# Performance work log

Hardware: AMD Instinct MI355X
Metric: run time of the kernel (lower is better)

The kernel has to match this reference:

```python
import jax, jax.numpy as jnp
import numpy as np

B, H, L, K = 4096, 2048, 16384, 32

def setup_inputs() -> dict:
    key = jax.random.key(0)
    k1, k2, k3 = jax.random.split(key, 3)
    x = jax.random.normal(k1, (B, H), dtype=jnp.float32)
    W_enc = jax.random.normal(k2, (L, H), dtype=jnp.float32) * (1.0 / np.sqrt(H))
    W_dec = jax.random.normal(k3, (H, L), dtype=jnp.float32)
    # normalize_decoder(): unit norm along dim=0 (hidden axis), per latent column
    W_dec = W_dec / jnp.linalg.norm(W_dec, axis=0, keepdims=True)
    return {"x": x, "W_enc": W_enc, "W_dec": W_dec, "topk": K}

def reference(x, W_enc, W_dec, topk):
    # encoder: z = relu(x @ W_enc^T)   [B, L]
    z_pre = jnp.einsum('bh,lh->bl', x, W_enc)
    z_relu = jax.nn.relu(z_pre)
    # top-k along last dim, scatter values into zeros (sparse latent code)
    vals, idx = jax.lax.top_k(z_relu, topk)            # [B, K]
    rows = jnp.arange(z_relu.shape[0])[:, None]        # [B, 1]
    z = jnp.zeros_like(z_relu).at[rows, idx].set(vals)  # [B, L]
    # decoder: x_hat = z @ W_dec^T    [B, H]
    x_hat = jnp.einsum('bl,hl->bh', z, W_dec)
    return (x_hat, z)
```

## Files before the change

kernel.cpp:

```cpp
#include <hip/hip_runtime.h>

#define B_ROWS 4096
#define H_DIM  2048
#define L_DIM  16384
#define TOPK   32
#define CAND_CAP 512
#define AMBIG_CAP 128
#define BAND 0.06f
#define ZP_STRIDE (2 * L_DIM)

typedef __attribute__((ext_vector_type(8))) short bf16x8;
typedef __attribute__((ext_vector_type(4))) float f32x4;

__device__ __forceinline__ unsigned short f32_to_bf16(float f) {
  unsigned int u = __float_as_uint(f);
  u += 0x7FFFu + ((u >> 16) & 1u);
  return (unsigned short)(u >> 16);
}
__device__ __forceinline__ float bf16_to_f32(unsigned short h) {
  return __uint_as_float(((unsigned int)h) << 16);
}

__device__ __forceinline__ void gload_lds16(const void* g, void* l) {
  __builtin_amdgcn_global_load_lds(
      (const __attribute__((address_space(1))) unsigned int*)g,
      (__attribute__((address_space(3))) unsigned int*)l, 16, 0, 0);
}

__global__ __launch_bounds__(256) void k_convert(const float* __restrict__ src,
                                                 unsigned short* __restrict__ dst, int n4) {
  int i = blockIdx.x * 256 + threadIdx.x;
  if (i < n4) {
    float4 v = ((const float4*)src)[i];
    ushort4 o;
    o.x = f32_to_bf16(v.x); o.y = f32_to_bf16(v.y);
    o.z = f32_to_bf16(v.z); o.w = f32_to_bf16(v.w);
    ((ushort4*)dst)[i] = o;
  }
}

__global__ __launch_bounds__(256) void k_transpose(const float* __restrict__ Wd,
                                                   unsigned short* __restrict__ WdT) {
  __shared__ float tile[64][65];
  int bi = blockIdx.x & 255;
  int bj = blockIdx.x >> 8;
  int t = threadIdx.x;
  int l0 = bi * 64, h0 = bj * 64;
#pragma unroll
  for (int p = 0; p < 4; ++p) {
    int hr = p * 16 + (t >> 4);
    int lc = (t & 15) * 4;
    float4 v = *(const float4*)(Wd + (size_t)(h0 + hr) * L_DIM + l0 + lc);
    tile[lc + 0][hr] = v.x; tile[lc + 1][hr] = v.y;
    tile[lc + 2][hr] = v.z; tile[lc + 3][hr] = v.w;
  }
  __syncthreads();
#pragma unroll
  for (int p = 0; p < 2; ++p) {
    int lr = p * 32 + (t >> 3);
    int hc = (t & 7) * 8;
    bf16x8 o;
#pragma unroll
    for (int i = 0; i < 8; ++i) o[i] = (short)f32_to_bf16(tile[lr][hc + i]);
    *(bf16x8*)(WdT + (size_t)(l0 + lr) * H_DIM + h0 + hc) = o;
  }
}

__global__ __launch_bounds__(512, 2) void k_gemm(const unsigned short* __restrict__ A,
                                                 const unsigned short* __restrict__ Bm,
                                                 unsigned short* __restrict__ Zp) {
  __shared__ unsigned short As[3 * 8192];
  __shared__ unsigned short Bs[3 * 8192];
  const size_t K = H_DIM;
  int bid = blockIdx.x;
  int cpx = gridDim.x >> 3;
  int swz = (bid & 7) * cpx + (bid >> 3);
  int tm = swz >> 6;
  int tn = swz & 63;
  int t = threadIdx.x;
  int lane = t & 63;
  int w = t >> 6;
  int wm = w >> 2, wn = w & 3;

  int rloc = lane & 15;
  int kc = lane >> 4;
  int swzk = (kc ^ ((rloc >> 1) & 3)) << 3;

  int srow = t >> 2;
  int kcs = (t & 3) ^ ((srow >> 1) & 3);
  const unsigned short* aS0 = A + (size_t)(tm * 256 + srow) * K + kcs * 8;
  const unsigned short* aS1 = aS0 + 128 * K;
  const unsigned short* bS0 = Bm + (size_t)(tn * 256 + srow) * K + kcs * 8;
  const unsigned short* bS1 = bS0 + 128 * K;
  int dA = t * 8;

  f32x4 acc[8][4];
#pragma unroll
  for (int i = 0; i < 8; ++i)
#pragma unroll
    for (int j = 0; j < 4; ++j) { f32x4 z = {0.f, 0.f, 0.f, 0.f}; acc[i][j] = z; }

#define STAGE_A(kt, sw) { size_t ko = (size_t)(kt) * 32; \
    gload_lds16(aS0 + ko, &As[(sw) * 8192 + dA]); \
    gload_lds16(aS1 + ko, &As[(sw) * 8192 + 4096 + dA]); }
#define STAGE_B(kt, sw) { size_t ko = (size_t)(kt) * 32; \
    gload_lds16(bS0 + ko, &Bs[(sw) * 8192 + dA]); \
    gload_lds16(bS1 + ko, &Bs[(sw) * 8192 + 4096 + dA]); }

  STAGE_A(0, 0) STAGE_B(0, 0)
  STAGE_A(1, 1) STAGE_B(1, 1)
  asm volatile("s_waitcnt vmcnt(4)" ::: "memory");
  __builtin_amdgcn_s_barrier();

  int sR = 0;
  const int aBase0 = (wm * 128 + rloc) * 32 + swzk;
  const int bBase0 = (wn * 64 + rloc) * 32 + swzk;
  const int NKT = H_DIM / 32;
  for (int kt = 0; kt < NKT; ++kt) {
    int sW = sR + 2; if (sW >= 3) sW -= 3;
    const unsigned short* Ab = &As[sR * 8192 + aBase0];
    const unsigned short* Bb = &Bs[sR * 8192 + bBase0];
    bool st = (kt + 2 < NKT);
    bf16x8 a0[4], b0[4];
#pragma unroll
    for (int m = 0; m < 4; ++m) a0[m] = *(const bf16x8*)(Ab + m * 512);
#pragma unroll
    for (int n = 0; n < 4; ++n) b0[n] = *(const bf16x8*)(Bb + n * 512);
    if (st) STAGE_A(kt + 2, sW)
    __builtin_amdgcn_s_barrier();
    __builtin_amdgcn_s_setprio(1);
#pragma unroll
    for (int m = 0; m < 4; ++m)
#pragma unroll
      for (int n = 0; n < 4; ++n)
        acc[m][n] = __builtin_amdgcn_mfma_f32_16x16x32_bf16(a0[m], b0[n], acc[m][n], 0, 0, 0);
    __builtin_amdgcn_s_setprio(0);
    __builtin_amdgcn_s_barrier();
    bf16x8 a1[4];
#pragma unroll
    for (int m = 0; m < 4; ++m) a1[m] = *(const bf16x8*)(Ab + (m + 4) * 512);
    if (st) STAGE_B(kt + 2, sW)
    __builtin_amdgcn_s_barrier();
    __builtin_amdgcn_s_setprio(1);
#pragma unroll
    for (int m = 0; m < 4; ++m)
#pragma unroll
      for (int n = 0; n < 4; ++n)
        acc[m + 4][n] = __builtin_amdgcn_mfma_f32_16x16x32_bf16(a1[m], b0[n], acc[m + 4][n], 0, 0, 0);
    __builtin_amdgcn_s_setprio(0);
    if (kt < NKT - 2) { asm volatile("s_waitcnt vmcnt(4)" ::: "memory"); }
    else if (kt == NKT - 2) { asm volatile("s_waitcnt vmcnt(0)" ::: "memory"); }
    __builtin_amdgcn_s_barrier();
    ++sR; if (sR == 3) sR = 0;
  }
#undef STAGE_A
#undef STAGE_B
  int colg = lane & 15, quad = lane >> 4;
  size_t rbase = (size_t)(tm * 256 + wm * 128 + quad * 4);
  int cbase = tn * 256 + wn * 64 + colg;
#pragma unroll
  for (int m = 0; m < 8; ++m)
#pragma unroll
    for (int n = 0; n < 4; ++n) {
      size_t rr = rbase + m * 16;
      int cc = cbase + n * 16;
#pragma unroll
      for (int r = 0; r < 4; ++r)
        Zp[(rr + r) * ZP_STRIDE + cc] = f32_to_bf16(fmaxf(acc[m][n][r], 0.0f));
    }
}

__global__ __launch_bounds__(256) void k_finish(const float* __restrict__ x,
                                                const float* __restrict__ Wenc,
                                                const unsigned short* __restrict__ WdT,
                                                float* __restrict__ zout,
                                                float* __restrict__ xhat) {
  int b = blockIdx.x;
  int t = threadIdx.x;
  __shared__ float xr[H_DIM];
  __shared__ float cv[CAND_CAP];
  __shared__ int   ci[CAND_CAP];
  __shared__ float s_b32;
  __shared__ unsigned int s_cnt, s_na, s_nin;
  __shared__ int    ai[AMBIG_CAP];
  __shared__ double ax[AMBIG_CAP];
  __shared__ float  sv[TOPK];
  __shared__ int    si[TOPK];

  const bf16x8* row = (const bf16x8*)((const unsigned short*)zout + (size_t)b * ZP_STRIDE);
  const float4* xv = (const float4*)(x + (size_t)b * H_DIM);
  for (int i = t; i < H_DIM / 4; i += 256) ((float4*)xr)[i] = xv[i];

  float thr = 2.3f;
  for (int attempt = 0; attempt < 8; ++attempt) {
    if (t == 0) s_cnt = 0;
    __syncthreads();
    for (int i = t; i < L_DIM / 8; i += 256) {
      bf16x8 v = row[i];
#pragma unroll
      for (int q = 0; q < 8; ++q) {
        float f = bf16_to_f32((unsigned short)v[q]);
        if (f > thr) {
          unsigned int p = atomicAdd(&s_cnt, 1u);
          if (p < CAND_CAP) { ci[p] = i * 8 + q; cv[p] = f; }
        }
      }
    }
    __syncthreads();
    if (s_cnt >= 40 || thr <= 0.0f) break;
    thr -= 0.6f; if (thr < 0.0f) thr = 0.0f;
    __syncthreads();
  }
  int cnt = (int)(s_cnt < CAND_CAP ? s_cnt : CAND_CAP);

  __syncthreads();
  {
    float4 zz = {0.f, 0.f, 0.f, 0.f};
    float4* zr = (float4*)(zout + (size_t)b * L_DIM);
#pragma unroll
    for (int i = 0; i < L_DIM / 4 / 256; ++i) zr[i * 256 + t] = zz;
  }
  if (t == 0) { s_b32 = -1.0f; s_na = 0; s_nin = 0; }
  __syncthreads();

  bool tiny = (cnt < TOPK);

  if (!tiny) {
    for (int i = t; i < cnt; i += 256) {
      float vi = cv[i]; int r = 0;
      for (int j = 0; j < cnt; ++j) { float vj = cv[j]; r += (vj > vi) || (vj == vi && j < i); }
      if (r == 31) s_b32 = vi;
    }
  }
  __syncthreads();
  float b32 = s_b32;

  if (!tiny) {
    for (int i = t; i < cnt; i += 256) {
      if (fabsf(cv[i] - b32) <= BAND) {
        unsigned int p = atomicAdd(&s_na, 1u);
        if (p < AMBIG_CAP) ai[p] = i;
      }
    }
  }
  __syncthreads();
  int na = (int)(s_na < AMBIG_CAP ? s_na : AMBIG_CAP);

  int wv = t >> 6, lane = t & 63;
  for (int a = wv; a < na; a += 4) {
    int l = ci[ai[a]];
    const float4* wrow = (const float4*)(Wenc + (size_t)l * H_DIM);
    double acc = 0.0;
#pragma unroll
    for (int k8 = 0; k8 < 8; ++k8) {
      float4 ww = wrow[k8 * 64 + lane];
      float4 xx = ((const float4*)xr)[k8 * 64 + lane];
      acc += (double)ww.x * xx.x + (double)ww.y * xx.y + (double)ww.z * xx.z + (double)ww.w * xx.w;
    }
#pragma unroll
    for (int s = 32; s; s >>= 1) acc += __shfl_xor(acc, s, 64);
    if (lane == 0) ax[a] = acc;
  }
  __syncthreads();

  for (int i = t; i < cnt; i += 256) {
    float vi = cv[i];
    if (tiny || vi - b32 > BAND) {
      unsigned int p = atomicAdd(&s_nin, 1u);
      sv[p] = vi; si[p] = ci[i];
      zout[(size_t)b * L_DIM + ci[i]] = vi;
    }
  }
  __syncthreads();
  int s0 = (int)s_nin;

  if (t < 64) {
    int need = TOPK - s0; if (need < 0) need = 0;
    for (int k = 0; k < need; ++k) {
      double bv = -1.0e300; int bidx = 0x7fffffff; int bpos = -1;
      for (int a = lane; a < na; a += 64) {
        double v = ax[a]; int ii = ci[ai[a]];
        if (v > bv || (v == bv && ii < bidx)) { bv = v; bidx = ii; bpos = a; }
      }
#pragma unroll
      for (int sh = 32; sh; sh >>= 1) {
        double ov = __shfl_xor(bv, sh, 64);
        int oi = __shfl_xor(bidx, sh, 64);
        int op = __shfl_xor(bpos, sh, 64);
        if (ov > bv || (ov == bv && oi < bidx)) { bv = ov; bidx = oi; bpos = op; }
      }
      bool valid = (bpos >= 0) && (bv > -1.0e299);
      if (lane == 0) {
        sv[s0 + k] = valid ? (float)bv : 0.0f;
        si[s0 + k] = valid ? bidx : 0;
        if (valid) zout[(size_t)b * L_DIM + bidx] = (float)bv;
      }
      for (int a = lane; a < na; a += 64) if (a == bpos) ax[a] = -1.0e300;
    }
  }
  __syncthreads();

  float acc[8] = {0.f, 0.f, 0.f, 0.f, 0.f, 0.f, 0.f, 0.f};
  for (int j = 0; j < TOPK; ++j) {
    float vj = sv[j];
    bf16x8 ww = *(const bf16x8*)(WdT + (size_t)si[j] * H_DIM + t * 8);
#pragma unroll
    for (int i = 0; i < 8; ++i) acc[i] += vj * bf16_to_f32((unsigned short)ww[i]);
  }
  float4 o0 = {acc[0], acc[1], acc[2], acc[3]};
  float4 o1 = {acc[4], acc[5], acc[6], acc[7]};
  float4* op = (float4*)(xhat + (size_t)b * H_DIM + t * 8);
  op[0] = o0; op[1] = o1;
}

extern "C" void kernel_launch(void* const* d_in, const int* in_sizes, int n_in,
                              void* d_out, int out_size, void* d_ws, size_t ws_size,
                              hipStream_t stream) {
  const float* x    = (const float*)d_in[0];
  const float* Wenc = (const float*)d_in[1];
  const float* Wdec = (const float*)d_in[2];

  float* xhat = (float*)d_out;
  float* z    = (float*)d_out + (size_t)B_ROWS * H_DIM;

  char* ws = (char*)d_ws;
  if (ws_size < 150994944u) return;
  unsigned short* xbf    = (unsigned short*)(ws);
  unsigned short* Wencbf = (unsigned short*)(ws + 16777216);
  unsigned short* WdT    = (unsigned short*)(ws + 83886080);

  unsigned short* zpre = (unsigned short*)z;

  k_convert<<<(2097152 + 255) / 256, 256, 0, stream>>>(x, xbf, 2097152);
  k_convert<<<(8388608 + 255) / 256, 256, 0, stream>>>(Wenc, Wencbf, 8388608);
  k_transpose<<<8192, 256, 0, stream>>>(Wdec, WdT);
  k_gemm<<<1024, 512, 0, stream>>>(xbf, Wencbf, zpre);
  k_finish<<<B_ROWS, 256, 0, stream>>>(x, Wenc, WdT, z, xhat);
}
```

Before: 641.0 us.

## Restructure GEMM main loop to 64-wide K tiles with four-phase double buffering

The encoder GEMM now stages 64-element K tiles (32 iterations instead of 64) into a single 128KB LDS buffer, with A and B each double-buffered and an 8-way XOR swizzle. Each iteration is split into four MFMA quadrants, and global-to-LDS loads for A (next tile) and B (tile after next) are interleaved between barriers. The aim is fewer barriers and loop overheads per FLOP and better overlap of loads with MFMA work. In exchange, LDS use grows to 128KB per block, which likely limits occupancy to one block per CU despite launch_bounds(512,2).

Result: faster. 580.1 us (-9.5%).

```diff
diff --git a/kernel.cpp b/kernel.cpp
--- a/kernel.cpp
+++ b/kernel.cpp
@@ -8,6 +8,7 @@
 #define AMBIG_CAP 128
 #define BAND 0.06f
 #define ZP_STRIDE (2 * L_DIM)
+#define NKT 32
 
 typedef __attribute__((ext_vector_type(8))) short bf16x8;
 typedef __attribute__((ext_vector_type(4))) float f32x4;
@@ -69,8 +70,7 @@
 __global__ __launch_bounds__(512, 2) void k_gemm(const unsigned short* __restrict__ A,
                                                  const unsigned short* __restrict__ Bm,
                                                  unsigned short* __restrict__ Zp) {
-  __shared__ unsigned short As[3 * 8192];
-  __shared__ unsigned short Bs[3 * 8192];
+  __shared__ unsigned short SL[65536];
   const size_t K = H_DIM;
   int bid = blockIdx.x;
   int cpx = gridDim.x >> 3;
@@ -84,15 +84,17 @@
 
   int rloc = lane & 15;
   int kc = lane >> 4;
-  int swzk = (kc ^ ((rloc >> 1) & 3)) << 3;
-
-  int srow = t >> 2;
-  int kcs = (t & 3) ^ ((srow >> 1) & 3);
-  const unsigned short* aS0 = A + (size_t)(tm * 256 + srow) * K + kcs * 8;
-  const unsigned short* aS1 = aS0 + 128 * K;
-  const unsigned short* bS0 = Bm + (size_t)(tn * 256 + srow) * K + kcs * 8;
-  const unsigned short* bS1 = bS0 + 128 * K;
-  int dA = t * 8;
+  int sw = rloc & 7;
+  int ck0 = ((kc) ^ sw) << 3;
+  int ck1 = ((4 + kc) ^ sw) << 3;
+  int arow = (wm * 128 + rloc) << 6;
+  int brow = (wn * 64 + rloc) << 6;
+
+  int srow = t >> 3;
+  int scs = ((t & 7) ^ (srow & 7)) << 3;
+  const unsigned short* aS = A  + (size_t)(tm * 256 + srow) * K + scs;
+  const unsigned short* bS = Bm + (size_t)(tn * 256 + srow) * K + scs;
+  int dst = t * 8;
 
   f32x4 acc[8][4];
 #pragma unroll
@@ -100,61 +102,97 @@
 #pragma unroll
     for (int j = 0; j < 4; ++j) { f32x4 z = {0.f, 0.f, 0.f, 0.f}; acc[i][j] = z; }
 
-#define STAGE_A(kt, sw) { size_t ko = (size_t)(kt) * 32; \
-    gload_lds16(aS0 + ko, &As[(sw) * 8192 + dA]); \
-    gload_lds16(aS1 + ko, &As[(sw) * 8192 + 4096 + dA]); }
-#define STAGE_B(kt, sw) { size_t ko = (size_t)(kt) * 32; \
-    gload_lds16(bS0 + ko, &Bs[(sw) * 8192 + dA]); \
-    gload_lds16(bS1 + ko, &Bs[(sw) * 8192 + 4096 + dA]); }
-
-  STAGE_A(0, 0) STAGE_B(0, 0)
-  STAGE_A(1, 1) STAGE_B(1, 1)
+#define SAU(kt, h, bf) { const unsigned short* s = aS + (size_t)(h) * 128 * K + (size_t)(kt) * 64; \
+    gload_lds16(s,          &SL[(bf) * 16384 + (h) * 8192 + dst]); \
+    gload_lds16(s + 64 * K, &SL[(bf) * 16384 + (h) * 8192 + 4096 + dst]); }
+#define SBU(kt, h, bf) { const unsigned short* s = bS + (size_t)(h) * 128 * K + (size_t)(kt) * 64; \
+    gload_lds16(s,          &SL[32768 + (bf) * 16384 + (h) * 8192 + dst]); \
+    gload_lds16(s + 64 * K, &SL[32768 + (bf) * 16384 + (h) * 8192 + 4096 + dst]); }
+
+  SAU(0, 0, 0) SAU(0, 1, 0) SBU(0, 0, 0) SBU(0, 1, 0) SBU(1, 0, 1) SBU(1, 1, 1)
   asm volatile("s_waitcnt vmcnt(4)" ::: "memory");
   __builtin_amdgcn_s_barrier();
 
-  int sR = 0;
-  const int aBase0 = (wm * 128 + rloc) * 32 + swzk;
-  const int bBase0 = (wn * 64 + rloc) * 32 + swzk;
-  const int NKT = H_DIM / 32;
-  for (int kt = 0; kt < NKT; ++kt) {
-    int sW = sR + 2; if (sW >= 3) sW -= 3;
-    const unsigned short* Ab = &As[sR * 8192 + aBase0];
-    const unsigned short* Bb = &Bs[sR * 8192 + bBase0];
-    bool st = (kt + 2 < NKT);
-    bf16x8 a0[4], b0[4];
-#pragma unroll
-    for (int m = 0; m < 4; ++m) a0[m] = *(const bf16x8*)(Ab + m * 512);
-#pragma unroll
-    for (int n = 0; n < 4; ++n) b0[n] = *(const bf16x8*)(Bb + n * 512);
-    if (st) STAGE_A(kt + 2, sW)
+  for (int tt = 0; tt < NKT; ++tt) {
+    int bf = tt & 1;
+    int ab = bf * 16384;
+    int bb = 32768 + ab;
+    bool stA = (tt + 1 < NKT);
+    bool stB = (tt + 2 < NKT);
+    bf16x8 a[4][2], b[4][2];
+#pragma unroll
+    for (int m = 0; m < 4; ++m) {
+      a[m][0] = *(const bf16x8*)&SL[ab + arow + m * 1024 + ck0];
+      a[m][1] = *(const bf16x8*)&SL[ab + arow + m * 1024 + ck1];
+    }
+#pragma unroll
+    for (int n = 0; n < 2; ++n) {
+      b[n][0] = *(const bf16x8*)&SL[bb + brow + n * 1024 + ck0];
+      b[n][1] = *(const bf16x8*)&SL[bb + brow + n * 1024 + ck1];
+    }
+    if (stA) SAU(tt + 1, 0, bf ^ 1)
     __builtin_amdgcn_s_barrier();
     __builtin_amdgcn_s_setprio(1);
 #pragma unroll
-    for (int m = 0; m < 4; ++m)
-#pragma unroll
-      for (int n = 0; n < 4; ++n)
-        acc[m][n] = __builtin_amdgcn_mfma_f32_16x16x32_bf16(a0[m], b0[n], acc[m][n], 0, 0, 0);
+    for (int kk = 0; kk < 2; ++kk)
+#pragma unroll
+      for (int m = 0; m < 4; ++m)
+#pragma unroll
+        for (int n = 0; n < 2; ++n)
+          acc[m][n] = __builtin_amdgcn_mfma_f32_16x16x32_bf16(a[m][kk], b[n][kk], acc[m][n], 0, 0, 0);
     __builtin_amdgcn_s_setprio(0);
     __builtin_amdgcn_s_barrier();
-    bf16x8 a1[4];
-#pragma unroll
-    for (int m = 0; m < 4; ++m) a1[m] = *(const bf16x8*)(Ab + (m + 4) * 512);
-    if (st) STAGE_B(kt + 2, sW)
+#pragma unroll
+    for (int n = 2; n < 4; ++n) {
+      b[n][0] = *(const bf16x8*)&SL[bb + brow + n * 1024 + ck0];
+      b[n][1] = *(const bf16x8*)&SL[bb + brow + n * 1024 + ck1];
+    }
+    if (stA) SAU(tt + 1, 1, bf ^ 1)
     __builtin_amdgcn_s_barrier();
     __builtin_amdgcn_s_setprio(1);
 #pragma unroll
-    for (int m = 0; m < 4; ++m)
-#pragma unroll
-      for (int n = 0; n < 4; ++n)
-        acc[m + 4][n] = __builtin_amdgcn_mfma_f32_16x16x32_bf16(a1[m], b0[n], acc[m + 4][n], 0, 0, 0);
+    for (int kk = 0; kk < 2; ++kk)
+#pragma unroll
+      for (int m = 0; m < 4; ++m)
+#pragma unroll
+        for (int n = 2; n < 4; ++n)
+          acc[m][n] = __builtin_amdgcn_mfma_f32_16x16x32_bf16(a[m][kk], b[n][kk], acc[m][n], 0, 0, 0);
     __builtin_amdgcn_s_setprio(0);
-    if (kt < NKT - 2) { asm volatile("s_waitcnt vmcnt(4)" ::: "memory"); }
-    else if (kt == NKT - 2) { asm volatile("s_waitcnt vmcnt(0)" ::: "memory"); }
-    __builtin_amdgcn_s_barrier();
-    ++sR; if (sR == 3) sR = 0;
-  }
-#undef STAGE_A
-#undef STAGE_B
+    __builtin_amdgcn_s_barrier();
+#pragma unroll
+    for (int m = 0; m < 4; ++m) {
+      a[m][0] = *(const bf16x8*)&SL[ab + arow + (m + 4) * 1024 + ck0];
+      a[m][1] = *(const bf16x8*)&SL[ab + arow + (m + 4) * 1024 + ck1];
+    }
+    if (stB) SBU(tt + 2, 0, bf)
+    __builtin_amdgcn_s_barrier();
+    __builtin_amdgcn_s_setprio(1);
+#pragma unroll
+    for (int kk = 0; kk < 2; ++kk)
+#pragma unroll
+      for (int m = 0; m < 4; ++m)
+#pragma unroll
+        for (int n = 0; n < 2; ++n)
+          acc[m + 4][n] = __builtin_amdgcn_mfma_f32_16x16x32_bf16(a[m][kk], b[n][kk], acc[m + 4][n], 0, 0, 0);
+    __builtin_amdgcn_s_setprio(0);
+    __builtin_amdgcn_s_barrier();
+    if (stB) SBU(tt + 2, 1, bf)
+    __builtin_amdgcn_s_barrier();
+    __builtin_amdgcn_s_setprio(1);
+#pragma unroll
+    for (int kk = 0; kk < 2; ++kk)
+#pragma unroll
+      for (int m = 0; m < 4; ++m)
+#pragma unroll
+        for (int n = 2; n < 4; ++n)
+          acc[m + 4][n] = __builtin_amdgcn_mfma_f32_16x16x32_bf16(a[m][kk], b[n][kk], acc[m + 4][n], 0, 0, 0);
+    __builtin_amdgcn_s_setprio(0);
+    if (tt < NKT - 2)       { asm volatile("s_waitcnt vmcnt(4)" ::: "memory"); }
+    else if (tt == NKT - 2) { asm volatile("s_waitcnt vmcnt(0)" ::: "memory"); }
+    __builtin_amdgcn_s_barrier();
+  }
+#undef SAU
+#undef SBU
   int colg = lane & 15, quad = lane >> 4;
   size_t rbase = (size_t)(tm * 256 + wm * 128 + quad * 4);
   int cbase = tn * 256 + wn * 64 + colg;
```
